# Performance work log

Hardware: AMD Instinct MI355X
Metric: run time of the kernel (lower is better)

Reference implementation:

```python
import jax, jax.numpy as jnp
import numpy as np

B, S, D_IN, D_H = 4, 2048, 1024, 1024

def setup_inputs() -> dict:
    key = jax.random.key(0)
    kx, kq, kk, kv = jax.random.split(key, 4)
    # nn.Linear default init: U(-1/sqrt(fan_in), 1/sqrt(fan_in)); stored as [out, in]
    bound = 1.0 / np.sqrt(D_IN)
    x = jax.random.normal(kx, (B, S, D_IN), dtype=jnp.float32)
    W_q = jax.random.uniform(kq, (D_H, D_IN), jnp.float32, -bound, bound)
    W_k = jax.random.uniform(kk, (D_H, D_IN), jnp.float32, -bound, bound)
    W_v = jax.random.uniform(kv, (D_H, D_IN), jnp.float32, -bound, bound)
    return {"x": x, "W_q": W_q, "W_k": W_k, "W_v": W_v}

def reference(x, W_q, W_k, W_v):
    # Q = x @ W_q.T, etc. (nn.Linear with bias=False)
    Q = jnp.einsum('bsd,hd->bsh', x, W_q)
    K = jnp.einsum('bsd,hd->bsh', x, W_k)
    V = jnp.einsum('bsd,hd->bsh', x, W_v)
    # NOTE: original scales by sqrt(Q.shape[1]) == sqrt(seq_len), not sqrt(d)
    scale = 1.0 / jnp.sqrt(jnp.asarray(Q.shape[1], Q.dtype))
    scores = jnp.einsum('bqh,bkh->bqk', Q, K) * scale  # [B,S,S]
    attn = jax.nn.softmax(scores, axis=-1)
    return jnp.einsum('bqk,bkh->bqh', attn, V)
```

## Files before the change

### kernel.cpp

```cpp
#include <hip/hip_runtime.h>

typedef unsigned short ushort_t;
typedef __attribute__((ext_vector_type(8))) __bf16 bf16x8;
typedef __attribute__((ext_vector_type(4))) float floatx4;

__device__ __forceinline__ ushort_t f2bf(float f) {
    unsigned int u = __builtin_bit_cast(unsigned int, f);
    u = (u + 0x7fffu + ((u >> 16) & 1u)) >> 16;
    return (ushort_t)u;
}

__device__ __forceinline__ int sw(int row, int cg) {
    return ((row << 2) + ((cg ^ row ^ (row >> 2)) & 3)) << 3;
}

__device__ __forceinline__ void gemm_core_pf(
    const ushort_t* __restrict__ A, int lda,
    const ushort_t* __restrict__ B, int ldb,
    int K, int tile_m, int tile_n,
    ushort_t* As, ushort_t* Bs,
    floatx4 (&acc)[4][4]) {

    const int tid  = threadIdx.x;
    const int lane = tid & 63;
    const int wave = tid >> 6;
    const int wm   = wave >> 1, wn = wave & 1;
    const int quad = lane >> 4;
    const int l16  = lane & 15;

#pragma unroll
    for (int i = 0; i < 4; i++)
#pragma unroll
        for (int j = 0; j < 4; j++) acc[i][j] = (floatx4){0.f, 0.f, 0.f, 0.f};

    const int s0 = tid, s1 = tid + 256;
    const int r0 = s0 >> 2, c0 = (s0 ^ r0 ^ (r0 >> 2)) & 3;
    const int r1 = s1 >> 2, c1 = (s1 ^ r1 ^ (r1 >> 2)) & 3;
    const ushort_t* ga0 = A + (long)(r0 + tile_m) * lda + c0 * 8;
    const ushort_t* ga1 = A + (long)(r1 + tile_m) * lda + c1 * 8;
    const ushort_t* gb0 = B + (long)(r0 + tile_n) * ldb + c0 * 8;
    const ushort_t* gb1 = B + (long)(r1 + tile_n) * ldb + c1 * 8;

    const int nk = K >> 5;

    bf16x8 ra0 = *(const bf16x8*)ga0;
    bf16x8 ra1 = *(const bf16x8*)ga1;
    bf16x8 rb0 = *(const bf16x8*)gb0;
    bf16x8 rb1 = *(const bf16x8*)gb1;
    *(bf16x8*)&As[s0 * 8] = ra0;
    *(bf16x8*)&As[s1 * 8] = ra1;
    *(bf16x8*)&Bs[s0 * 8] = rb0;
    *(bf16x8*)&Bs[s1 * 8] = rb1;
    __syncthreads();

    for (int ks = 0; ks < nk; ++ks) {
        const int cur = ks & 1, nxt = cur ^ 1;

        if (ks + 1 < nk) {
            const int k1 = (ks + 1) << 5;
            ra0 = *(const bf16x8*)(ga0 + k1);
            ra1 = *(const bf16x8*)(ga1 + k1);
            rb0 = *(const bf16x8*)(gb0 + k1);
            rb1 = *(const bf16x8*)(gb1 + k1);
        }

        const ushort_t* as = &As[cur * 4096];
        const ushort_t* bs = &Bs[cur * 4096];
        bf16x8 af[4], bfr[4];
#pragma unroll
        for (int im = 0; im < 4; im++)
            af[im] = *(const bf16x8*)&as[sw(wm * 64 + im * 16 + l16, quad)];
#pragma unroll
        for (int in = 0; in < 4; in++)
            bfr[in] = *(const bf16x8*)&bs[sw(wn * 64 + in * 16 + l16, quad)];
#pragma unroll
        for (int im = 0; im < 4; im++)
#pragma unroll
            for (int in = 0; in < 4; in++)
                acc[im][in] = __builtin_amdgcn_mfma_f32_16x16x32_bf16(
                    af[im], bfr[in], acc[im][in], 0, 0, 0);

        if (ks + 1 < nk) {
            *(bf16x8*)&As[nxt * 4096 + s0 * 8] = ra0;
            *(bf16x8*)&As[nxt * 4096 + s1 * 8] = ra1;
            *(bf16x8*)&Bs[nxt * 4096 + s0 * 8] = rb0;
            *(bf16x8*)&Bs[nxt * 4096 + s1 * 8] = rb1;
            __syncthreads();
        }
    }
}

__global__ void cvt_kernel(const float* __restrict__ x,
                           const float* __restrict__ wq,
                           const float* __restrict__ wk,
                           const float* __restrict__ wv,
                           ushort_t* __restrict__ dst,
                           float* __restrict__ lsum) {
    if (blockIdx.x >= 11264) {
        int idx = (blockIdx.x - 11264) * 256 + threadIdx.x;
        ((float4*)lsum)[idx] = (float4){0.f, 0.f, 0.f, 0.f};
        return;
    }
    const long NX = 8388608, NW = 1048576;
    long g = ((long)blockIdx.x * blockDim.x + threadIdx.x) * 4;
    const float* src;
    long off;
    if (g < NX)             { src = x;  off = g; }
    else if (g < NX + NW)   { src = wq; off = g - NX; }
    else if (g < NX + 2*NW) { src = wk; off = g - NX - NW; }
    else                    { src = wv; off = g - NX - 2*NW; }
    float4 v = *(const float4*)(src + off);
    ushort4 o;
    o.x = f2bf(v.x); o.y = f2bf(v.y); o.z = f2bf(v.z); o.w = f2bf(v.w);
    *(ushort4*)(dst + g) = o;
}

__global__ __launch_bounds__(256) void qkv_kernel(
    const ushort_t* __restrict__ xb,
    const ushort_t* __restrict__ wqb,
    const ushort_t* __restrict__ wkb,
    const ushort_t* __restrict__ wvb,
    ushort_t* __restrict__ Qb,
    ushort_t* __restrict__ Kb,
    ushort_t* __restrict__ VTb) {

    __shared__ __align__(16) ushort_t As[2 * 128 * 32];
    __shared__ __align__(16) ushort_t Bs[2 * 128 * 32];

    const int z = blockIdx.z;
    const ushort_t *A, *B;
    ushort_t* C;
    int ldc, tile_m, tile_n;
    if (z == 2) {
        A = wvb; B = xb; C = VTb; ldc = 8192;
        tile_m = blockIdx.x * 128; tile_n = blockIdx.y * 128;
    } else {
        A = xb; B = z ? wkb : wqb; C = z ? Kb : Qb; ldc = 1024;
        tile_m = blockIdx.y * 128; tile_n = blockIdx.x * 128;
    }

    floatx4 acc[4][4];
    gemm_core_pf(A, 1024, B, 1024, 1024, tile_m, tile_n, As, Bs, acc);

    const int lane = threadIdx.x & 63, wave = threadIdx.x >> 6;
    const int wm = wave >> 1, wn = wave & 1, quad = lane >> 4, l16 = lane & 15;
#pragma unroll
    for (int im = 0; im < 4; im++)
#pragma unroll
        for (int r = 0; r < 4; r++) {
            int row = tile_m + wm * 64 + im * 16 + quad * 4 + r;
#pragma unroll
            for (int in = 0; in < 4; in++) {
                int col = tile_n + wn * 64 + in * 16 + l16;
                C[(long)row * ldc + col] = f2bf(acc[im][in][r]);
            }
        }
}

__global__ __launch_bounds__(256) void pexp_kernel(
    const ushort_t* __restrict__ Qb,
    const ushort_t* __restrict__ Kb,
    ushort_t* __restrict__ Pb,
    float* __restrict__ lsum) {

    __shared__ __align__(16) ushort_t As[2 * 128 * 32];
    __shared__ __align__(16) ushort_t Bs[2 * 128 * 32];

    const int z = blockIdx.z;
    const ushort_t* A = Qb + (long)z * 2097152;
    const ushort_t* B = Kb + (long)z * 2097152;
    ushort_t* C = Pb + (long)z * 4194304;
    float* l = lsum + z * 2048;
    const int tile_m = blockIdx.y * 128;
    const int tile_n = blockIdx.x * 128;

    floatx4 acc[4][4];
    gemm_core_pf(A, 1024, B, 1024, 1024, tile_m, tile_n, As, Bs, acc);

    const float scale = 0.022097086912079608f;
    const int lane = threadIdx.x & 63, wave = threadIdx.x >> 6;
    const int wm = wave >> 1, wn = wave & 1, quad = lane >> 4, l16 = lane & 15;
#pragma unroll
    for (int im = 0; im < 4; im++)
#pragma unroll
        for (int r = 0; r < 4; r++) {
            int row = tile_m + wm * 64 + im * 16 + quad * 4 + r;
            float psum = 0.f;
#pragma unroll
            for (int in = 0; in < 4; in++) {
                int col = tile_n + wn * 64 + in * 16 + l16;
                float e = __expf(acc[im][in][r] * scale);
                C[(long)row * 2048 + col] = f2bf(e);
                psum += e;
            }
            psum += __shfl_xor(psum, 1, 64);
            psum += __shfl_xor(psum, 2, 64);
            psum += __shfl_xor(psum, 4, 64);
            psum += __shfl_xor(psum, 8, 64);
            if (l16 == 0) atomicAdd(&l[row], psum);
        }
}

__global__ __launch_bounds__(256) void out_kernel(
    const ushort_t* __restrict__ Pb,
    const ushort_t* __restrict__ VTb,
    float* __restrict__ out,
    const float* __restrict__ lsum) {

    __shared__ __align__(16) ushort_t As[2 * 128 * 32];
    __shared__ __align__(16) ushort_t Bs[2 * 128 * 32];

    const int z = blockIdx.z;
    const ushort_t* A = Pb + (long)z * 4194304;
    const ushort_t* B = VTb + (long)z * 2048;
    float* C = out + (long)z * 2097152;
    const float* l = lsum + z * 2048;
    const int tile_m = blockIdx.y * 128;
    const int tile_n = blockIdx.x * 128;

    floatx4 acc[4][4];
    gemm_core_pf(A, 2048, B, 8192, 2048, tile_m, tile_n, As, Bs, acc);

    const int lane = threadIdx.x & 63, wave = threadIdx.x >> 6;
    const int wm = wave >> 1, wn = wave & 1, quad = lane >> 4, l16 = lane & 15;
#pragma unroll
    for (int im = 0; im < 4; im++)
#pragma unroll
        for (int r = 0; r < 4; r++) {
            int row = tile_m + wm * 64 + im * 16 + quad * 4 + r;
            float li = 1.0f / l[row];
#pragma unroll
            for (int in = 0; in < 4; in++) {
                int col = tile_n + wn * 64 + in * 16 + l16;
                C[(long)row * 1024 + col] = acc[im][in][r] * li;
            }
        }
}

extern "C" void kernel_launch(void* const* d_in, const int* in_sizes, int n_in,
                              void* d_out, int out_size, void* d_ws, size_t ws_size,
                              hipStream_t stream) {
    const float* x  = (const float*)d_in[0];
    const float* wq = (const float*)d_in[1];
    const float* wk = (const float*)d_in[2];
    const float* wv = (const float*)d_in[3];

    ushort_t* xb  = (ushort_t*)d_ws;
    ushort_t* wqb = xb  + 8388608;
    ushort_t* wkb = wqb + 1048576;
    ushort_t* wvb = wkb + 1048576;
    ushort_t* Qb  = wvb + 1048576;
    ushort_t* Kb  = Qb  + 8388608;
    ushort_t* VTb = Kb  + 8388608;
    ushort_t* Pb  = VTb + 8388608;
    float*    lsum = (float*)(Pb + 16777216);
    float*    out  = (float*)d_out;

    cvt_kernel<<<11272, 256, 0, stream>>>(x, wq, wk, wv, xb, lsum);

    qkv_kernel<<<dim3(8, 64, 3), 256, 0, stream>>>(xb, wqb, wkb, wvb, Qb, Kb, VTb);

    pexp_kernel<<<dim3(16, 16, 4), 256, 0, stream>>>(Qb, Kb, Pb, lsum);

    out_kernel<<<dim3(8, 16, 4), 256, 0, stream>>>(Pb, VTb, out, lsum);
}
```

Baseline: 272.5 us.

## Fold Wq and Wk into one Gram matrix to drop a projection GEMM

Precomputes G = Wk^T·Wq from transposed bf16 weights, then forms Y = x·G^T so scores become Y·x^T. This replaces separate Q and K projections over all tokens with one token-sized GEMM plus a small 1024×1024 GEMM. The GEMM core is templated on tile sizes so the small GEMM can use 64×64 tiles. It adds two extra kernel launches (transpose and G) and an extra bf16 rounding of G, which may affect accuracy.

```diff
diff --git a/kernel.cpp b/kernel.cpp
--- a/kernel.cpp
+++ b/kernel.cpp
@@ -14,12 +14,16 @@
     return ((row << 2) + ((cg ^ row ^ (row >> 2)) & 3)) << 3;
 }
 
+template <int BM, int BN, int IM, int IN>
 __device__ __forceinline__ void gemm_core_pf(
     const ushort_t* __restrict__ A, int lda,
     const ushort_t* __restrict__ B, int ldb,
     int K, int tile_m, int tile_n,
     ushort_t* As, ushort_t* Bs,
-    floatx4 (&acc)[4][4]) {
+    floatx4 (&acc)[IM][IN]) {
+
+    constexpr int SA = BM * 4 / 256;
+    constexpr int SB = BN * 4 / 256;
 
     const int tid  = threadIdx.x;
     const int lane = tid & 63;
@@ -29,28 +33,40 @@
     const int l16  = lane & 15;
 
 #pragma unroll
-    for (int i = 0; i < 4; i++)
-#pragma unroll
-        for (int j = 0; j < 4; j++) acc[i][j] = (floatx4){0.f, 0.f, 0.f, 0.f};
-
-    const int s0 = tid, s1 = tid + 256;
-    const int r0 = s0 >> 2, c0 = (s0 ^ r0 ^ (r0 >> 2)) & 3;
-    const int r1 = s1 >> 2, c1 = (s1 ^ r1 ^ (r1 >> 2)) & 3;
-    const ushort_t* ga0 = A + (long)(r0 + tile_m) * lda + c0 * 8;
-    const ushort_t* ga1 = A + (long)(r1 + tile_m) * lda + c1 * 8;
-    const ushort_t* gb0 = B + (long)(r0 + tile_n) * ldb + c0 * 8;
-    const ushort_t* gb1 = B + (long)(r1 + tile_n) * ldb + c1 * 8;
+    for (int i = 0; i < IM; i++)
+#pragma unroll
+        for (int j = 0; j < IN; j++) acc[i][j] = (floatx4){0.f, 0.f, 0.f, 0.f};
+
+    const ushort_t* ga[SA];
+    int la[SA];
+#pragma unroll
+    for (int s = 0; s < SA; s++) {
+        int seg = tid + s * 256;
+        int r = seg >> 2, c = (seg ^ r ^ (r >> 2)) & 3;
+        ga[s] = A + (long)(r + tile_m) * lda + c * 8;
+        la[s] = seg * 8;
+    }
+    const ushort_t* gb[SB];
+    int lb[SB];
+#pragma unroll
+    for (int s = 0; s < SB; s++) {
+        int seg = tid + s * 256;
+        int r = seg >> 2, c = (seg ^ r ^ (r >> 2)) & 3;
+        gb[s] = B + (long)(r + tile_n) * ldb + c * 8;
+        lb[s] = seg * 8;
+    }
 
     const int nk = K >> 5;
 
-    bf16x8 ra0 = *(const bf16x8*)ga0;
-    bf16x8 ra1 = *(const bf16x8*)ga1;
-    bf16x8 rb0 = *(const bf16x8*)gb0;
-    bf16x8 rb1 = *(const bf16x8*)gb1;
-    *(bf16x8*)&As[s0 * 8] = ra0;
-    *(bf16x8*)&As[s1 * 8] = ra1;
-    *(bf16x8*)&Bs[s0 * 8] = rb0;
-    *(bf16x8*)&Bs[s1 * 8] = rb1;
+    bf16x8 ra[SA], rb[SB];
+#pragma unroll
+    for (int s = 0; s < SA; s++) ra[s] = *(const bf16x8*)ga[s];
+#pragma unroll
+    for (int s = 0; s < SB; s++) rb[s] = *(const bf16x8*)gb[s];
+#pragma unroll
+    for (int s = 0; s < SA; s++) *(bf16x8*)&As[la[s]] = ra[s];
+#pragma unroll
+    for (int s = 0; s < SB; s++) *(bf16x8*)&Bs[lb[s]] = rb[s];
     __syncthreads();
 
     for (int ks = 0; ks < nk; ++ks) {
@@ -58,70 +74,118 @@
 
         if (ks + 1 < nk) {
             const int k1 = (ks + 1) << 5;
-            ra0 = *(const bf16x8*)(ga0 + k1);
-            ra1 = *(const bf16x8*)(ga1 + k1);
-            rb0 = *(const bf16x8*)(gb0 + k1);
-            rb1 = *(const bf16x8*)(gb1 + k1);
-        }
-
-        const ushort_t* as = &As[cur * 4096];
-        const ushort_t* bs = &Bs[cur * 4096];
-        bf16x8 af[4], bfr[4];
-#pragma unroll
-        for (int im = 0; im < 4; im++)
-            af[im] = *(const bf16x8*)&as[sw(wm * 64 + im * 16 + l16, quad)];
-#pragma unroll
-        for (int in = 0; in < 4; in++)
-            bfr[in] = *(const bf16x8*)&bs[sw(wn * 64 + in * 16 + l16, quad)];
-#pragma unroll
-        for (int im = 0; im < 4; im++)
-#pragma unroll
-            for (int in = 0; in < 4; in++)
+#pragma unroll
+            for (int s = 0; s < SA; s++) ra[s] = *(const bf16x8*)(ga[s] + k1);
+#pragma unroll
+            for (int s = 0; s < SB; s++) rb[s] = *(const bf16x8*)(gb[s] + k1);
+        }
+
+        const ushort_t* as = &As[cur * BM * 32];
+        const ushort_t* bs = &Bs[cur * BN * 32];
+        bf16x8 af[IM], bfr[IN];
+#pragma unroll
+        for (int im = 0; im < IM; im++)
+            af[im] = *(const bf16x8*)&as[sw(wm * IM * 16 + im * 16 + l16, quad)];
+#pragma unroll
+        for (int in = 0; in < IN; in++)
+            bfr[in] = *(const bf16x8*)&bs[sw(wn * IN * 16 + in * 16 + l16, quad)];
+#pragma unroll
+        for (int im = 0; im < IM; im++)
+#pragma unroll
+            for (int in = 0; in < IN; in++)
                 acc[im][in] = __builtin_amdgcn_mfma_f32_16x16x32_bf16(
                     af[im], bfr[in], acc[im][in], 0, 0, 0);
 
         if (ks + 1 < nk) {
-            *(bf16x8*)&As[nxt * 4096 + s0 * 8] = ra0;
-            *(bf16x8*)&As[nxt * 4096 + s1 * 8] = ra1;
-            *(bf16x8*)&Bs[nxt * 4096 + s0 * 8] = rb0;
-            *(bf16x8*)&Bs[nxt * 4096 + s1 * 8] = rb1;
+#pragma unroll
+            for (int s = 0; s < SA; s++) *(bf16x8*)&As[nxt * BM * 32 + la[s]] = ra[s];
+#pragma unroll
+            for (int s = 0; s < SB; s++) *(bf16x8*)&Bs[nxt * BN * 32 + lb[s]] = rb[s];
             __syncthreads();
         }
     }
 }
 
 __global__ void cvt_kernel(const float* __restrict__ x,
-                           const float* __restrict__ wq,
-                           const float* __restrict__ wk,
                            const float* __restrict__ wv,
-                           ushort_t* __restrict__ dst,
+                           ushort_t* __restrict__ xb,
+                           ushort_t* __restrict__ wvb,
                            float* __restrict__ lsum) {
-    if (blockIdx.x >= 11264) {
-        int idx = (blockIdx.x - 11264) * 256 + threadIdx.x;
+    const int bx = blockIdx.x;
+    if (bx >= 9216) {
+        int idx = (bx - 9216) * 256 + threadIdx.x;
         ((float4*)lsum)[idx] = (float4){0.f, 0.f, 0.f, 0.f};
         return;
     }
-    const long NX = 8388608, NW = 1048576;
-    long g = ((long)blockIdx.x * blockDim.x + threadIdx.x) * 4;
     const float* src;
-    long off;
-    if (g < NX)             { src = x;  off = g; }
-    else if (g < NX + NW)   { src = wq; off = g - NX; }
-    else if (g < NX + 2*NW) { src = wk; off = g - NX - NW; }
-    else                    { src = wv; off = g - NX - 2*NW; }
-    float4 v = *(const float4*)(src + off);
+    ushort_t* dst;
+    long g;
+    if (bx < 8192) { src = x;  dst = xb;  g = ((long)bx * 256 + threadIdx.x) * 4; }
+    else           { src = wv; dst = wvb; g = ((long)(bx - 8192) * 256 + threadIdx.x) * 4; }
+    float4 v = *(const float4*)(src + g);
     ushort4 o;
     o.x = f2bf(v.x); o.y = f2bf(v.y); o.z = f2bf(v.z); o.w = f2bf(v.w);
     *(ushort4*)(dst + g) = o;
 }
 
-__global__ __launch_bounds__(256) void qkv_kernel(
+__global__ void tkern(const float* __restrict__ wq, const float* __restrict__ wk,
+                      ushort_t* __restrict__ wqT, ushort_t* __restrict__ wkT) {
+    const float* src = blockIdx.z ? wk : wq;
+    ushort_t* dst = blockIdx.z ? wkT : wqT;
+    __shared__ ushort_t tile[64 * 80];
+
+    const int t = threadIdx.x;
+    const int h0 = blockIdx.y * 64, d0 = blockIdx.x * 64;
+    {
+        int i = t >> 2, cg = (t & 3) << 4;
+        const float4* p = (const float4*)(src + (long)(h0 + i) * 1024 + d0 + cg);
+#pragma unroll
+        for (int k = 0; k < 4; k++) {
+            float4 v = p[k];
+            ushort_t* q = &tile[i * 80 + cg + k * 4];
+            q[0] = f2bf(v.x); q[1] = f2bf(v.y); q[2] = f2bf(v.z); q[3] = f2bf(v.w);
+        }
+    }
+    __syncthreads();
+    {
+        int j = t >> 2, ig = (t & 3) << 4;
+        ushort_t tmp[16];
+#pragma unroll
+        for (int k = 0; k < 16; k++) tmp[k] = tile[(ig + k) * 80 + j];
+        ushort_t* o = dst + (long)(d0 + j) * 1024 + h0 + ig;
+        *(uint4*)o = ((uint4*)tmp)[0];
+        *(uint4*)(o + 8) = ((uint4*)tmp)[1];
+    }
+}
+
+__global__ __launch_bounds__(256) void ggemm_kernel(
+    const ushort_t* __restrict__ wkT, const ushort_t* __restrict__ wqT,
+    ushort_t* __restrict__ G) {
+    __shared__ __align__(16) ushort_t As[2 * 64 * 32];
+    __shared__ __align__(16) ushort_t Bs[2 * 64 * 32];
+    const int tile_m = blockIdx.y * 64, tile_n = blockIdx.x * 64;
+    floatx4 acc[2][2];
+    gemm_core_pf<64, 64, 2, 2>(wkT, 1024, wqT, 1024, 1024, tile_m, tile_n, As, Bs, acc);
+    const int lane = threadIdx.x & 63, wave = threadIdx.x >> 6;
+    const int wm = wave >> 1, wn = wave & 1, quad = lane >> 4, l16 = lane & 15;
+#pragma unroll
+    for (int im = 0; im < 2; im++)
+#pragma unroll
+        for (int r = 0; r < 4; r++) {
+            int row = tile_m + wm * 32 + im * 16 + quad * 4 + r;
+#pragma unroll
+            for (int in = 0; in < 2; in++) {
+                int col = tile_n + wn * 32 + in * 16 + l16;
+                G[(long)row * 1024 + col] = f2bf(acc[im][in][r]);
+            }
+        }
+}
+
+__global__ __launch_bounds__(256) void yv_kernel(
     const ushort_t* __restrict__ xb,
-    const ushort_t* __restrict__ wqb,
-    const ushort_t* __restrict__ wkb,
+    const ushort_t* __restrict__ Gb,
     const ushort_t* __restrict__ wvb,
-    ushort_t* __restrict__ Qb,
-    ushort_t* __restrict__ Kb,
+    ushort_t* __restrict__ Yb,
     ushort_t* __restrict__ VTb) {
 
     __shared__ __align__(16) ushort_t As[2 * 128 * 32];
@@ -131,16 +195,16 @@
     const ushort_t *A, *B;
     ushort_t* C;
     int ldc, tile_m, tile_n;
-    if (z == 2) {
+    if (z == 0) {
+        A = xb; B = Gb; C = Yb; ldc = 1024;
+        tile_m = blockIdx.y * 128; tile_n = blockIdx.x * 128;
+    } else {
         A = wvb; B = xb; C = VTb; ldc = 8192;
         tile_m = blockIdx.x * 128; tile_n = blockIdx.y * 128;
-    } else {
-        A = xb; B = z ? wkb : wqb; C = z ? Kb : Qb; ldc = 1024;
-        tile_m = blockIdx.y * 128; tile_n = blockIdx.x * 128;
     }
 
     floatx4 acc[4][4];
-    gemm_core_pf(A, 1024, B, 1024, 1024, tile_m, tile_n, As, Bs, acc);
+    gemm_core_pf<128, 128, 4, 4>(A, 1024, B, 1024, 1024, tile_m, tile_n, As, Bs, acc);
 
     const int lane = threadIdx.x & 63, wave = threadIdx.x >> 6;
     const int wm = wave >> 1, wn = wave & 1, quad = lane >> 4, l16 = lane & 15;
@@ -158,8 +222,8 @@
 }
 
 __global__ __launch_bounds__(256) void pexp_kernel(
-    const ushort_t* __restrict__ Qb,
-    const ushort_t* __restrict__ Kb,
+    const ushort_t* __restrict__ Yb,
+    const ushort_t* __restrict__ xb,
     ushort_t* __restrict__ Pb,
     float* __restrict__ lsum) {
 
@@ -167,15 +231,15 @@
     __shared__ __align__(16) ushort_t Bs[2 * 128 * 32];
 
     const int z = blockIdx.z;
-    const ushort_t* A = Qb + (long)z * 2097152;
-    const ushort_t* B = Kb + (long)z * 2097152;
+    const ushort_t* A = Yb + (long)z * 2097152;
+    const ushort_t* B = xb + (long)z * 2097152;
     ushort_t* C = Pb + (long)z * 4194304;
     float* l = lsum + z * 2048;
     const int tile_m = blockIdx.y * 128;
     const int tile_n = blockIdx.x * 128;
 
     floatx4 acc[4][4];
-    gemm_core_pf(A, 1024, B, 1024, 1024, tile_m, tile_n, As, Bs, acc);
+    gemm_core_pf<128, 128, 4, 4>(A, 1024, B, 1024, 1024, tile_m, tile_n, As, Bs, acc);
 
     const float scale = 0.022097086912079608f;
     const int lane = threadIdx.x & 63, wave = threadIdx.x >> 6;
@@ -219,7 +283,7 @@
     const int tile_n = blockIdx.x * 128;
 
     floatx4 acc[4][4];
-    gemm_core_pf(A, 2048, B, 8192, 2048, tile_m, tile_n, As, Bs, acc);
+    gemm_core_pf<128, 128, 4, 4>(A, 2048, B, 8192, 2048, tile_m, tile_n, As, Bs, acc);
 
     const int lane = threadIdx.x & 63, wave = threadIdx.x >> 6;
     const int wm = wave >> 1, wn = wave & 1, quad = lane >> 4, l16 = lane & 15;
@@ -246,21 +310,25 @@
     const float* wv = (const float*)d_in[3];
 
     ushort_t* xb  = (ushort_t*)d_ws;
-    ushort_t* wqb = xb  + 8388608;
-    ushort_t* wkb = wqb + 1048576;
-    ushort_t* wvb = wkb + 1048576;
-    ushort_t* Qb  = wvb + 1048576;
-    ushort_t* Kb  = Qb  + 8388608;
-    ushort_t* VTb = Kb  + 8388608;
+    ushort_t* wvb = xb  + 8388608;
+    ushort_t* wqT = wvb + 1048576;
+    ushort_t* wkT = wqT + 1048576;
+    ushort_t* Gb  = wkT + 1048576;
+    ushort_t* Yb  = Gb  + 1048576;
+    ushort_t* VTb = Yb  + 8388608;
     ushort_t* Pb  = VTb + 8388608;
     float*    lsum = (float*)(Pb + 16777216);
     float*    out  = (float*)d_out;
 
-    cvt_kernel<<<11272, 256, 0, stream>>>(x, wq, wk, wv, xb, lsum);
-
-    qkv_kernel<<<dim3(8, 64, 3), 256, 0, stream>>>(xb, wqb, wkb, wvb, Qb, Kb, VTb);
-
-    pexp_kernel<<<dim3(16, 16, 4), 256, 0, stream>>>(Qb, Kb, Pb, lsum);
+    cvt_kernel<<<9224, 256, 0, stream>>>(x, wv, xb, wvb, lsum);
+
+    tkern<<<dim3(16, 16, 2), 256, 0, stream>>>(wq, wk, wqT, wkT);
+
+    ggemm_kernel<<<dim3(16, 16), 256, 0, stream>>>(wkT, wqT, Gb);
+
+    yv_kernel<<<dim3(8, 64, 2), 256, 0, stream>>>(xb, Gb, wvb, Yb, VTb);
+
+    pexp_kernel<<<dim3(16, 16, 4), 256, 0, stream>>>(Yb, xb, Pb, lsum);
 
     out_kernel<<<dim3(8, 16, 4), 256, 0, stream>>>(Pb, VTb, out, lsum);
 }
```

Result: no change. 269.8 us (-1.0%).
